# Kernel tuning notes

Measured on AMD Instinct MI355X. Metric: run time of the kernel, lower is better.

Reference implementation:

```python
import jax, jax.numpy as jnp
import numpy as np

N = 50000   # nodes
E = 300000  # directed edges (~Delaunay mesh, degree 6)
H = 128     # hidden_size
TW = 5      # time_window
P = 3       # process_steps
NODE_IN = 9
EDGE_IN = 4
LN_EPS = 1e-5


def _ln(x, g, b):
    m = jnp.mean(x, axis=-1, keepdims=True)
    v = jnp.var(x, axis=-1, keepdims=True)
    return (x - m) * jax.lax.rsqrt(v + LN_EPS) * g + b


def _mlp_ln(x, w1, b1, w2, b2, g, bb):
    # Linear -> ReLU -> Linear -> LayerNorm (matches MLP(..., layer_norm=True))
    h = jax.nn.relu(x @ w1 + b1)
    return _ln(h @ w2 + b2, g, bb)


def setup_inputs() -> dict:
    key = jax.random.key(0)
    ks = iter(jax.random.split(key, 64))
    def nrm(shape):
        return jax.random.normal(next(ks), shape, jnp.float32)
    def lin(fi, fo, stack=None):
        sh = (fi, fo) if stack is None else (stack, fi, fo)
        return nrm(sh) / np.sqrt(fi)
    inp = {}
    inp["temperature"] = nrm((N,))
    inp["temperature_prev"] = nrm((N,))
    inp["heat_source"] = nrm((N,))
    inp["heat_source_prev"] = nrm((N,))
    inp["heat_source_next"] = nrm((N, TW))
    inp["mesh_pos"] = jax.random.uniform(next(ks), (N, 2), jnp.float32)
    inp["edge_index"] = jax.random.randint(next(ks), (2, E), 0, N, jnp.int32)
    # Normalizer params (running mean/std)
    inp["node_norm_mean"] = jnp.zeros((NODE_IN,), jnp.float32)
    inp["node_norm_std"] = jnp.ones((NODE_IN,), jnp.float32)
    inp["edge_norm_mean"] = jnp.zeros((EDGE_IN,), jnp.float32)
    inp["edge_norm_std"] = jnp.ones((EDGE_IN,), jnp.float32)
    # node encoder
    inp["ne_w1"] = lin(NODE_IN, H); inp["ne_b1"] = jnp.zeros((H,), jnp.float32)
    inp["ne_w2"] = lin(H, H);       inp["ne_b2"] = jnp.zeros((H,), jnp.float32)
    inp["ne_g"] = jnp.ones((H,), jnp.float32); inp["ne_be"] = jnp.zeros((H,), jnp.float32)
    # edge encoder
    inp["ee_w1"] = lin(EDGE_IN, H); inp["ee_b1"] = jnp.zeros((H,), jnp.float32)
    inp["ee_w2"] = lin(H, H);       inp["ee_b2"] = jnp.zeros((H,), jnp.float32)
    inp["ee_g"] = jnp.ones((H,), jnp.float32); inp["ee_be"] = jnp.zeros((H,), jnp.float32)
    # processors (stacked over P steps): edge_mlp in=3H, node_mlp in=2H
    inp["pe_w1"] = lin(3 * H, H, P); inp["pe_b1"] = jnp.zeros((P, H), jnp.float32)
    inp["pe_w2"] = lin(H, H, P);     inp["pe_b2"] = jnp.zeros((P, H), jnp.float32)
    inp["pe_g"] = jnp.ones((P, H), jnp.float32); inp["pe_be"] = jnp.zeros((P, H), jnp.float32)
    inp["pn_w1"] = lin(2 * H, H, P); inp["pn_b1"] = jnp.zeros((P, H), jnp.float32)
    inp["pn_w2"] = lin(H, H, P);     inp["pn_b2"] = jnp.zeros((P, H), jnp.float32)
    inp["pn_g"] = jnp.ones((P, H), jnp.float32); inp["pn_be"] = jnp.zeros((P, H), jnp.float32)
    # decoder (Conv1d kernel_size=1 == per-node Linear), Swish in between
    inp["dec_w1"] = lin(H, H // 2); inp["dec_b1"] = jnp.zeros((H // 2,), jnp.float32)
    inp["dec_w2"] = lin(H // 2, TW); inp["dec_b2"] = jnp.zeros((TW,), jnp.float32)
    return inp


def reference(temperature, temperature_prev, heat_source, heat_source_prev,
              heat_source_next, mesh_pos, edge_index,
              node_norm_mean, node_norm_std, edge_norm_mean, edge_norm_std,
              ne_w1, ne_b1, ne_w2, ne_b2, ne_g, ne_be,
              ee_w1, ee_b1, ee_w2, ee_b2, ee_g, ee_be,
              pe_w1, pe_b1, pe_w2, pe_b2, pe_g, pe_be,
              pn_w1, pn_b1, pn_w2, pn_b2, pn_g, pn_be,
              dec_w1, dec_b1, dec_w2, dec_b2):
    u = temperature
    # node features: [u, u_dot, q, q_dot, q_next]  -> [N, 9]
    x = jnp.concatenate([
        u[:, None], (u - temperature_prev)[:, None],
        heat_source[:, None], (heat_source - heat_source_prev)[:, None],
        heat_source_next], axis=-1)
    s, r = edge_index[0], edge_index[1]  # senders (source j), receivers (target i)
    rel = mesh_pos[s] - mesh_pos[r]                       # [E, 2]
    dist = jnp.linalg.norm(rel, axis=-1, keepdims=True)   # [E, 1]
    relt = (u[s] - u[r])[:, None]                         # [E, 1]
    e = jnp.concatenate([rel, dist, relt], axis=-1)       # [E, 4]

    xh = _mlp_ln((x - node_norm_mean) / node_norm_std, ne_w1, ne_b1, ne_w2, ne_b2, ne_g, ne_be)
    eh = _mlp_ln((e - edge_norm_mean) / edge_norm_std, ee_w1, ee_b1, ee_w2, ee_b2, ee_g, ee_be)

    n_nodes = xh.shape[0]
    for i in range(P):
        xs, xr = xh[s], xh[r]  # x_j = x[source], x_i = x[target]
        # message: edge_mlp(cat[x_i, x_j, e]) then scatter-add at target index
        msg = _mlp_ln(jnp.concatenate([xr, xs, eh], axis=-1),
                      pe_w1[i], pe_b1[i], pe_w2[i], pe_b2[i], pe_g[i], pe_be[i])
        aggr = jax.ops.segment_sum(msg, r, num_segments=n_nodes)
        # node update + residual
        new_x = _mlp_ln(jnp.concatenate([aggr, xh], axis=-1),
                        pn_w1[i], pn_b1[i], pn_w2[i], pn_b2[i], pn_g[i], pn_be[i]) + xh
        # edge update (note row/col ordering differs from message) + residual
        new_e = _mlp_ln(jnp.concatenate([xs, xr, eh], axis=-1),
                        pe_w1[i], pe_b1[i], pe_w2[i], pe_b2[i], pe_g[i], pe_be[i]) + eh
        xh, eh = new_x, new_e

    # decoder: 1x1 convs == per-node linears, Swish(beta=1) activation
    h = xh @ dec_w1 + dec_b1
    h = h * jax.nn.sigmoid(h)
    delta = (h @ dec_w2 + dec_b2).reshape(-1, TW)
    dt = jnp.arange(1, TW + 1, dtype=delta.dtype)
    return dt[None, :] * delta
```

## Files before the change

kernel.cpp:

```cpp
#include <hip/hip_runtime.h>
#include <stdint.h>

typedef unsigned short u16;
typedef __attribute__((ext_vector_type(8))) short bf16x8_t;
typedef __attribute__((ext_vector_type(4))) float f32x4_t;

__device__ __forceinline__ float bl(u16 x) {
  union { unsigned u; float f; } c; c.u = ((unsigned)x) << 16; return c.f;
}
__device__ __forceinline__ u16 fb(float x) {
  union { float f; unsigned u; } c; c.f = x;
  unsigned r = c.u + 0x7fffu + ((c.u >> 16) & 1u);
  return (u16)(r >> 16);
}

__global__ void sentinel_kernel(float* out, int n) {
  int i = blockIdx.x * 256 + threadIdx.x;
  if (i < n) out[i] = 12345.f;
}

struct TSeg { const float* src; u16* dst; };
struct TArgs { TSeg s[23]; };
__global__ void transpose_w(TArgs a) {
  __shared__ u16 sT[128][132];
  const float* src = a.s[blockIdx.x].src;
  u16* dst = a.s[blockIdx.x].dst;
  for (int e = threadIdx.x; e < 16384; e += 256) {
    int k = e >> 7, n = e & 127;
    sT[n][k] = fb(src[e]);
  }
  __syncthreads();
  for (int e = threadIdx.x; e < 16384; e += 256) {
    int n = e >> 7, k = e & 127;
    dst[e] = sT[n][k];
  }
}

__global__ void zero_i32(int* p, int n) {
  int i = blockIdx.x * 256 + threadIdx.x;
  if (i < n) p[i] = 0;
}
__global__ void deg_count(const int* __restrict__ ei, int* __restrict__ cnt, int E) {
  int e = blockIdx.x * 256 + threadIdx.x;
  if (e < E) atomicAdd(&cnt[ei[E + e]], 1);
}
__global__ void scan1(const int* __restrict__ cnt, int* __restrict__ part,
                      int* __restrict__ bsum, int N) {
  __shared__ int s[256];
  int i = blockIdx.x * 256 + threadIdx.x;
  s[threadIdx.x] = (i < N) ? cnt[i] : 0;
  __syncthreads();
#pragma unroll
  for (int o = 1; o < 256; o <<= 1) {
    int t = (threadIdx.x >= o) ? s[threadIdx.x - o] : 0;
    __syncthreads();
    s[threadIdx.x] += t;
    __syncthreads();
  }
  if (i < N) part[i] = s[threadIdx.x];
  if (threadIdx.x == 255) bsum[blockIdx.x] = s[255];
}
__global__ void scan2(int* bsum, int nb) {
  __shared__ int s[256];
  __shared__ int carry;
  if (threadIdx.x == 0) carry = 0;
  __syncthreads();
  for (int base = 0; base < nb; base += 256) {
    int i = base + threadIdx.x;
    int v = (i < nb) ? bsum[i] : 0;
    s[threadIdx.x] = v;
    __syncthreads();
#pragma unroll
    for (int o = 1; o < 256; o <<= 1) {
      int t = (threadIdx.x >= o) ? s[threadIdx.x - o] : 0;
      __syncthreads();
      s[threadIdx.x] += t;
      __syncthreads();
    }
    int exc = s[threadIdx.x] - v + carry;
    if (i < nb) bsum[i] = exc;
    __syncthreads();
    if (threadIdx.x == 255) carry += s[255];
    __syncthreads();
  }
}
__global__ void scan3(const int* __restrict__ part, const int* __restrict__ bsum,
                      int* __restrict__ start, int N) {
  int i = blockIdx.x * 256 + threadIdx.x;
  if (i < N) start[i + 1] = part[i] + bsum[i >> 8];
  if (i == 0) start[0] = 0;
}
__global__ void fill_slot(const int* __restrict__ ei, int* __restrict__ cnt2,
                          const int* __restrict__ start, int* __restrict__ sortedS,
                          int* __restrict__ sortedR, int E) {
  int e = blockIdx.x * 256 + threadIdx.x;
  if (e >= E) return;
  int s = ei[e], r = ei[E + e];
  int p = atomicAdd(&cnt2[r], 1);
  int slot = start[r] + p;
  sortedS[slot] = s;
  sortedR[slot] = r;
}

__global__ void node_feat_kernel(const float* __restrict__ t, const float* __restrict__ tp,
                                 const float* __restrict__ q, const float* __restrict__ qp,
                                 const float* __restrict__ qn, const float* __restrict__ nm,
                                 const float* __restrict__ ns, float* __restrict__ nfeat,
                                 int n_nodes) {
  int n = blockIdx.x * 256 + threadIdx.x;
  if (n >= n_nodes) return;
  float u = t[n];
  float x[9];
  x[0] = u; x[1] = u - tp[n];
  float hq = q[n];
  x[2] = hq; x[3] = hq - qp[n];
#pragma unroll
  for (int j = 0; j < 5; ++j) x[4 + j] = qn[n * 5 + j];
#pragma unroll
  for (int k = 0; k < 9; ++k) nfeat[n * 9 + k] = (x[k] - nm[k]) / ns[k];
}

__global__ void edge_feat_kernel(const int* __restrict__ sArr, const int* __restrict__ rArr,
                                 const float* __restrict__ mp, const float* __restrict__ u,
                                 const float* __restrict__ em, const float* __restrict__ es,
                                 float* __restrict__ efeat, int n_edges) {
  int e = blockIdx.x * 256 + threadIdx.x;
  if (e >= n_edges) return;
  int s = sArr[e], r = rArr[e];
  float rx = mp[s * 2] - mp[r * 2];
  float ry = mp[s * 2 + 1] - mp[r * 2 + 1];
  float d = sqrtf(rx * rx + ry * ry);
  float rt = u[s] - u[r];
  float x[4] = {rx, ry, d, rt};
#pragma unroll
  for (int k = 0; k < 4; ++k) efeat[e * 4 + k] = (x[k] - em[k]) / es[k];
}

template <int K, bool DUAL>
__global__ __launch_bounds__(256, 2) void encode_fused(
    const float* __restrict__ feat, const float* __restrict__ w1f, const float* __restrict__ b1f,
    const u16* __restrict__ wt2, const float* __restrict__ b2, const float* __restrict__ gg,
    const float* __restrict__ bb, u16* __restrict__ out,
    const u16* __restrict__ wtA2, const u16* __restrict__ wtB2, u16* __restrict__ xhA,
    u16* __restrict__ xhB, float* __restrict__ aggr, int M) {
  __shared__ float sW1[K * 128];
  __shared__ float sB1[128];
  __shared__ u16 sH[64][136];
  __shared__ u16 sO1[DUAL ? 64 : 1][136];
  const int tid = threadIdx.x;
  const int wave = tid >> 6, lane = tid & 63;
  const int q = lane >> 4, l16 = lane & 15;
  const int m0 = blockIdx.x * 64;
  const int rowb = wave * 16 + q * 4;
  const int arow = m0 + wave * 16 + l16;
  const int arc = arow < M ? arow : M - 1;

  for (int i = tid; i < K * 128; i += 256) sW1[i] = w1f[i];
  if (tid < 128) sB1[tid] = b1f[tid];
  __syncthreads();

  float fr[K];
#pragma unroll
  for (int k = 0; k < K; ++k) fr[k] = feat[(size_t)arc * K + k];

  f32x4_t acc[8];
#pragma unroll
  for (int b = 0; b < 8; ++b) acc[b] = (f32x4_t){0.f, 0.f, 0.f, 0.f};
#pragma unroll
  for (int kk = 0; kk < 4; ++kk) {
    union { u16 u[8]; bf16x8_t v; } cv;
#pragma unroll
    for (int j = 0; j < 8; ++j) {
      int col = kk * 32 + q * 8 + j;
      float h = sB1[col];
#pragma unroll
      for (int k = 0; k < K; ++k) h += fr[k] * sW1[k * 128 + col];
      cv.u[j] = fb(h > 0.f ? h : 0.f);
    }
#pragma unroll
    for (int nt = 0; nt < 8; ++nt) {
      bf16x8_t bfv = *(const bf16x8_t*)(wt2 + (size_t)(nt * 16 + l16) * 128 + kk * 32 + q * 8);
      acc[nt] = __builtin_amdgcn_mfma_f32_16x16x32_bf16(cv.v, bfv, acc[nt], 0, 0, 0);
    }
  }

  float bcol[8], gcol[8], becol[8];
#pragma unroll
  for (int nt = 0; nt < 8; ++nt) {
    bcol[nt] = b2[nt * 16 + l16];
    gcol[nt] = gg[nt * 16 + l16];
    becol[nt] = bb[nt * 16 + l16];
  }
  float s[4] = {0, 0, 0, 0}, ss[4] = {0, 0, 0, 0};
#pragma unroll
  for (int r = 0; r < 4; ++r)
#pragma unroll
    for (int nt = 0; nt < 8; ++nt) {
      float v = acc[nt][r] + bcol[nt];
      s[r] += v;
      ss[r] += v * v;
    }
#pragma unroll
  for (int r = 0; r < 4; ++r) {
#pragma unroll
    for (int m = 1; m <= 8; m <<= 1) {
      s[r] += __shfl_xor(s[r], m, 64);
      ss[r] += __shfl_xor(ss[r], m, 64);
    }
  }
#pragma unroll
  for (int r = 0; r < 4; ++r) {
    float mean = s[r] * (1.f / 128.f);
    float var = fmaxf(ss[r] * (1.f / 128.f) - mean * mean, 0.f);
    float rstd = rsqrtf(var + 1e-5f);
#pragma unroll
    for (int nt = 0; nt < 8; ++nt) {
      float v = (acc[nt][r] + bcol[nt] - mean) * rstd * gcol[nt] + becol[nt];
      sH[rowb + r][nt * 16 + l16] = fb(v);
    }
  }
  __syncthreads();
#pragma unroll
  for (int it = 0; it < 4; ++it) {
    int lin = it * 256 + tid;
    int row = lin >> 4, ch = (lin & 15) * 8;
    int grow = m0 + row;
    if (grow >= M) continue;
    *(uint4*)(out + (size_t)grow * 128 + ch) = *(uint4*)(&sH[row][ch]);
  }

  if constexpr (DUAL) {
    {
      float4 z = make_float4(0.f, 0.f, 0.f, 0.f);
#pragma unroll
      for (int it = 0; it < 8; ++it) {
        int lin = it * 256 + tid;
        int row = lin >> 5, c4 = (lin & 31) * 4;
        int grow = m0 + row;
        if (grow < M) *(float4*)(aggr + (size_t)grow * 128 + c4) = z;
      }
    }
    f32x4_t a0[8], a1[8];
#pragma unroll
    for (int b = 0; b < 8; ++b) {
      a0[b] = (f32x4_t){0.f, 0.f, 0.f, 0.f};
      a1[b] = (f32x4_t){0.f, 0.f, 0.f, 0.f};
    }
#pragma unroll
    for (int kk = 0; kk < 4; ++kk) {
      bf16x8_t af = *(const bf16x8_t*)(&sH[wave * 16 + l16][kk * 32 + q * 8]);
#pragma unroll
      for (int nt = 0; nt < 8; ++nt) {
        bf16x8_t b0 = *(const bf16x8_t*)(wtA2 + (size_t)(nt * 16 + l16) * 128 + kk * 32 + q * 8);
        bf16x8_t b1v = *(const bf16x8_t*)(wtB2 + (size_t)(nt * 16 + l16) * 128 + kk * 32 + q * 8);
        a0[nt] = __builtin_amdgcn_mfma_f32_16x16x32_bf16(af, b0, a0[nt], 0, 0, 0);
        a1[nt] = __builtin_amdgcn_mfma_f32_16x16x32_bf16(af, b1v, a1[nt], 0, 0, 0);
      }
    }
    __syncthreads();
#pragma unroll
    for (int r = 0; r < 4; ++r)
#pragma unroll
      for (int nt = 0; nt < 8; ++nt) {
        sH[rowb + r][nt * 16 + l16] = fb(a0[nt][r]);
        sO1[rowb + r][nt * 16 + l16] = fb(a1[nt][r]);
      }
    __syncthreads();
#pragma unroll
    for (int it = 0; it < 4; ++it) {
      int lin = it * 256 + tid;
      int row = lin >> 4, ch = (lin & 15) * 8;
      int grow = m0 + row;
      if (grow >= M) continue;
      *(uint4*)(xhA + (size_t)grow * 128 + ch) = *(uint4*)(&sH[row][ch]);
      *(uint4*)(xhB + (size_t)grow * 128 + ch) = *(uint4*)(&sO1[row][ch]);
    }
  }
}

__global__ __launch_bounds__(256, 2) void node_fused_2w(
    u16* __restrict__ xh, float* __restrict__ aggr, const u16* __restrict__ wtA,
    const u16* __restrict__ wtB, const float* __restrict__ b1, const u16* __restrict__ wt2,
    const float* __restrict__ b2, const float* __restrict__ gg, const float* __restrict__ bb,
    const u16* __restrict__ wtA2, const u16* __restrict__ wtB2, u16* __restrict__ xhA,
    u16* __restrict__ xhB, int M) {
  __shared__ u16 sH[64][136];
  __shared__ u16 sO1[64][136];
  const int tid = threadIdx.x;
  const int wave = tid >> 6, lane = tid & 63;
  const int q = lane >> 4, l16 = lane & 15;
  const int m0 = blockIdx.x * 64;
  const int rowb = wave * 16 + q * 4;
  const int arow = m0 + wave * 16 + l16;
  const int arc = arow < M ? arow : M - 1;

  bf16x8_t xf[4], af_[4];
#pragma unroll
  for (int kk = 0; kk < 4; ++kk) {
    xf[kk] = *(const bf16x8_t*)(xh + (size_t)arc * 128 + kk * 32 + q * 8);
    const float* ap = aggr + (size_t)arc * 128 + kk * 32 + q * 8;
    union { u16 u[8]; bf16x8_t v; } cv;
#pragma unroll
    for (int j = 0; j < 8; ++j) cv.u[j] = fb(ap[j]);
    af_[kk] = cv.v;
  }

  f32x4_t acc[8];
#pragma unroll
  for (int b = 0; b < 8; ++b) acc[b] = (f32x4_t){0.f, 0.f, 0.f, 0.f};
#pragma unroll
  for (int kk = 0; kk < 4; ++kk) {
#pragma unroll
    for (int nt = 0; nt < 8; ++nt) {
      bf16x8_t bA = *(const bf16x8_t*)(wtA + (size_t)(nt * 16 + l16) * 128 + kk * 32 + q * 8);
      bf16x8_t bB = *(const bf16x8_t*)(wtB + (size_t)(nt * 16 + l16) * 128 + kk * 32 + q * 8);
      acc[nt] = __builtin_amdgcn_mfma_f32_16x16x32_bf16(af_[kk], bA, acc[nt], 0, 0, 0);
      acc[nt] = __builtin_amdgcn_mfma_f32_16x16x32_bf16(xf[kk], bB, acc[nt], 0, 0, 0);
    }
  }
  float bcol1[8];
#pragma unroll
  for (int nt = 0; nt < 8; ++nt) bcol1[nt] = b1[nt * 16 + l16];
#pragma unroll
  for (int r = 0; r < 4; ++r)
#pragma unroll
    for (int nt = 0; nt < 8; ++nt) {
      float v = acc[nt][r] + bcol1[nt];
      sH[rowb + r][nt * 16 + l16] = fb(v > 0.f ? v : 0.f);
    }
  __syncthreads();

  f32x4_t acc2[8];
#pragma unroll
  for (int b = 0; b < 8; ++b) acc2[b] = (f32x4_t){0.f, 0.f, 0.f, 0.f};
#pragma unroll
  for (int kk = 0; kk < 4; ++kk) {
    bf16x8_t afm = *(const bf16x8_t*)(&sH[wave * 16 + l16][kk * 32 + q * 8]);
#pragma unroll
    for (int nt = 0; nt < 8; ++nt) {
      bf16x8_t bfv = *(const bf16x8_t*)(wt2 + (size_t)(nt * 16 + l16) * 128 + kk * 32 + q * 8);
      acc2[nt] = __builtin_amdgcn_mfma_f32_16x16x32_bf16(afm, bfv, acc2[nt], 0, 0, 0);
    }
  }
  float bcol[8], gcol[8], becol[8];
#pragma unroll
  for (int nt = 0; nt < 8; ++nt) {
    bcol[nt] = b2[nt * 16 + l16];
    gcol[nt] = gg[nt * 16 + l16];
    becol[nt] = bb[nt * 16 + l16];
  }
  float s[4] = {0, 0, 0, 0}, ss[4] = {0, 0, 0, 0};
#pragma unroll
  for (int r = 0; r < 4; ++r)
#pragma unroll
    for (int nt = 0; nt < 8; ++nt) {
      float v = acc2[nt][r] + bcol[nt];
      s[r] += v;
      ss[r] += v * v;
    }
#pragma unroll
  for (int r = 0; r < 4; ++r) {
#pragma unroll
    for (int m = 1; m <= 8; m <<= 1) {
      s[r] += __shfl_xor(s[r], m, 64);
      ss[r] += __shfl_xor(ss[r], m, 64);
    }
  }
  __syncthreads();
#pragma unroll
  for (int r = 0; r < 4; ++r) {
    float mean = s[r] * (1.f / 128.f);
    float var = fmaxf(ss[r] * (1.f / 128.f) - mean * mean, 0.f);
    float rstd = rsqrtf(var + 1e-5f);
#pragma unroll
    for (int nt = 0; nt < 8; ++nt) {
      float v = (acc2[nt][r] + bcol[nt] - mean) * rstd * gcol[nt] + becol[nt];
      sH[rowb + r][nt * 16 + l16] = fb(v);
    }
  }
  __syncthreads();

  bf16x8_t nf[4];
#pragma unroll
  for (int kk = 0; kk < 4; ++kk) {
    u16 y8[8];
    *(uint4*)y8 = *(uint4*)(&sH[wave * 16 + l16][kk * 32 + q * 8]);
#pragma unroll
    for (int j = 0; j < 8; ++j) y8[j] = fb(bl(y8[j]) + bl((u16)xf[kk][j]));
    nf[kk] = *(bf16x8_t*)y8;
    if (arow < M)
      *(uint4*)(xh + (size_t)arow * 128 + kk * 32 + q * 8) = *(uint4*)y8;
  }

  if (wtA2 == nullptr) return;

  if (arow < M) {
    float4 z = make_float4(0.f, 0.f, 0.f, 0.f);
#pragma unroll
    for (int kk = 0; kk < 4; ++kk) {
      *(float4*)(aggr + (size_t)arow * 128 + kk * 32 + q * 8) = z;
      *(float4*)(aggr + (size_t)arow * 128 + kk * 32 + q * 8 + 4) = z;
    }
  }

  f32x4_t a0[8], a1[8];
#pragma unroll
  for (int b = 0; b < 8; ++b) {
    a0[b] = (f32x4_t){0.f, 0.f, 0.f, 0.f};
    a1[b] = (f32x4_t){0.f, 0.f, 0.f, 0.f};
  }
#pragma unroll
  for (int kk = 0; kk < 4; ++kk) {
#pragma unroll
    for (int nt = 0; nt < 8; ++nt) {
      bf16x8_t b0 = *(const bf16x8_t*)(wtA2 + (size_t)(nt * 16 + l16) * 128 + kk * 32 + q * 8);
      bf16x8_t b1v = *(const bf16x8_t*)(wtB2 + (size_t)(nt * 16 + l16) * 128 + kk * 32 + q * 8);
      a0[nt] = __builtin_amdgcn_mfma_f32_16x16x32_bf16(nf[kk], b0, a0[nt], 0, 0, 0);
      a1[nt] = __builtin_amdgcn_mfma_f32_16x16x32_bf16(nf[kk], b1v, a1[nt], 0, 0, 0);
    }
  }
  __syncthreads();
#pragma unroll
  for (int r = 0; r < 4; ++r)
#pragma unroll
    for (int nt = 0; nt < 8; ++nt) {
      sH[rowb + r][nt * 16 + l16] = fb(a0[nt][r]);
      sO1[rowb + r][nt * 16 + l16] = fb(a1[nt][r]);
    }
  __syncthreads();
#pragma unroll
  for (int it = 0; it < 4; ++it) {
    int lin = it * 256 + tid;
    int row = lin >> 4, ch = (lin & 15) * 8;
    int grow = m0 + row;
    if (grow >= M) continue;
    *(uint4*)(xhA + (size_t)grow * 128 + ch) = *(uint4*)(&sH[row][ch]);
    *(uint4*)(xhB + (size_t)grow * 128 + ch) = *(uint4*)(&sO1[row][ch]);
  }
}

template <bool CSR, bool LAST>
__global__ __launch_bounds__(256, 2) void edge_fused(
    u16* __restrict__ eh, const u16* __restrict__ xhA, const u16* __restrict__ xhB,
    const u16* __restrict__ wtC, const float* __restrict__ b1, const u16* __restrict__ wt2,
    const float* __restrict__ b2, const float* __restrict__ gg, const float* __restrict__ bb,
    const int* __restrict__ sArr, const int* __restrict__ rArr,
    const int* __restrict__ startp, float* __restrict__ aggr, int E) {
  __shared__ u16 sHm[64][136];
  __shared__ u16 sHe[LAST ? 1 : 64][136];
  __shared__ int sR[64];
  __shared__ float sB1[128];
  const int tid = threadIdx.x;
  const int wave = tid >> 6, lane = tid & 63;
  const int q = lane >> 4, l16 = lane & 15;
  const int m0 = blockIdx.x * 64;
  const int rowb = wave * 16 + q * 4;
  int arow = m0 + wave * 16 + l16;
  int arc = arow < E ? arow : E - 1;

  if (tid < 64) {
    int e = m0 + tid;
    sR[tid] = (e < E) ? rArr[e] : -1;
  }
  if (tid < 128) sB1[tid] = b1[tid];

  int psv[4], prv[4];
#pragma unroll
  for (int it = 0; it < 4; ++it) {
    int lin = it * 256 + tid;
    int ge = m0 + (lin >> 4);
    int gc = ge < E ? ge : E - 1;
    psv[it] = sArr[gc];
    prv[it] = rArr[gc];
  }

  bf16x8_t ehf[4];
#pragma unroll
  for (int kk = 0; kk < 4; ++kk)
    ehf[kk] = *(const bf16x8_t*)(eh + (size_t)arc * 128 + kk * 32 + q * 8);

  f32x4_t accC[8];
#pragma unroll
  for (int b = 0; b < 8; ++b) accC[b] = (f32x4_t){0.f, 0.f, 0.f, 0.f};
#pragma unroll
  for (int kk = 0; kk < 4; ++kk) {
#pragma unroll
    for (int nt = 0; nt < 8; ++nt) {
      bf16x8_t bfv = *(const bf16x8_t*)(wtC + (size_t)(nt * 16 + l16) * 128 + kk * 32 + q * 8);
      accC[nt] = __builtin_amdgcn_mfma_f32_16x16x32_bf16(ehf[kk], bfv, accC[nt], 0, 0, 0);
    }
  }
  __builtin_amdgcn_sched_barrier(0);

  uint4 pAr[4], pBs[4], pAs[4], pBr[4];
#pragma unroll
  for (int it = 0; it < 4; ++it) {
    int ch = ((it * 256 + tid) & 15) * 8;
    pAr[it] = *(const uint4*)(xhA + (size_t)prv[it] * 128 + ch);
    pBs[it] = *(const uint4*)(xhB + (size_t)psv[it] * 128 + ch);
    if constexpr (!LAST) {
      pAs[it] = *(const uint4*)(xhA + (size_t)psv[it] * 128 + ch);
      pBr[it] = *(const uint4*)(xhB + (size_t)prv[it] * 128 + ch);
    }
  }

#pragma unroll
  for (int r = 0; r < 4; ++r)
#pragma unroll
    for (int nt = 0; nt < 8; ++nt) sHm[rowb + r][nt * 16 + l16] = fb(accC[nt][r]);
  __syncthreads();

#pragma unroll
  for (int it = 0; it < 4; ++it) {
    int lin = it * 256 + tid;
    int row = lin >> 4, ch = (lin & 15) * 8;
    bool ok = (m0 + row) < E;
    u16 t8[8], ar[8], as_[8], br[8], bs[8], hm[8], he[8];
    *(uint4*)t8 = *(uint4*)(&sHm[row][ch]);
    *(uint4*)ar = pAr[it];
    *(uint4*)bs = pBs[it];
    if constexpr (!LAST) {
      *(uint4*)as_ = pAs[it];
      *(uint4*)br = pBr[it];
    }
#pragma unroll
    for (int j = 0; j < 8; ++j) {
      float t = bl(t8[j]) + sB1[ch + j];
      float vm = t + bl(ar[j]) + bl(bs[j]);
      hm[j] = (ok && vm > 0.f) ? fb(vm) : 0;
      if constexpr (!LAST) {
        float ve = t + bl(as_[j]) + bl(br[j]);
        he[j] = (ok && ve > 0.f) ? fb(ve) : 0;
      }
    }
    *(uint4*)(&sHm[row][ch]) = *(uint4*)hm;
    if constexpr (!LAST) *(uint4*)(&sHe[row][ch]) = *(uint4*)he;
  }
  __syncthreads();

  float bcol[8], gcol[8], becol[8];
#pragma unroll
  for (int nt = 0; nt < 8; ++nt) {
    bcol[nt] = b2[nt * 16 + l16];
    gcol[nt] = gg[nt * 16 + l16];
    becol[nt] = bb[nt * 16 + l16];
  }

  f32x4_t accM[8], accE[8];
#pragma unroll
  for (int b = 0; b < 8; ++b) {
    accM[b] = (f32x4_t){0.f, 0.f, 0.f, 0.f};
    accE[b] = (f32x4_t){0.f, 0.f, 0.f, 0.f};
  }
#pragma unroll
  for (int kk = 0; kk < 4; ++kk) {
    bf16x8_t afm = *(const bf16x8_t*)(&sHm[wave * 16 + l16][kk * 32 + q * 8]);
    bf16x8_t afe;
    if constexpr (!LAST) afe = *(const bf16x8_t*)(&sHe[wave * 16 + l16][kk * 32 + q * 8]);
#pragma unroll
    for (int nt = 0; nt < 8; ++nt) {
      bf16x8_t bfv = *(const bf16x8_t*)(wt2 + (size_t)(nt * 16 + l16) * 128 + kk * 32 + q * 8);
      accM[nt] = __builtin_amdgcn_mfma_f32_16x16x32_bf16(afm, bfv, accM[nt], 0, 0, 0);
      if constexpr (!LAST)
        accE[nt] = __builtin_amdgcn_mfma_f32_16x16x32_bf16(afe, bfv, accE[nt], 0, 0, 0);
    }
  }
  float sm[4] = {0, 0, 0, 0}, ssm[4] = {0, 0, 0, 0};
  float se[4] = {0, 0, 0, 0}, sse[4] = {0, 0, 0, 0};
#pragma unroll
  for (int r = 0; r < 4; ++r)
#pragma unroll
    for (int nt = 0; nt < 8; ++nt) {
      float vm = accM[nt][r] + bcol[nt];
      sm[r] += vm; ssm[r] += vm * vm;
      if constexpr (!LAST) {
        float ve = accE[nt][r] + bcol[nt];
        se[r] += ve; sse[r] += ve * ve;
      }
    }
#pragma unroll
  for (int r = 0; r < 4; ++r) {
#pragma unroll
    for (int m = 1; m <= 8; m <<= 1) {
      sm[r] += __shfl_xor(sm[r], m, 64);
      ssm[r] += __shfl_xor(ssm[r], m, 64);
      if constexpr (!LAST) {
        se[r] += __shfl_xor(se[r], m, 64);
        sse[r] += __shfl_xor(sse[r], m, 64);
      }
    }
  }

  if (!CSR) {
#pragma unroll
    for (int r = 0; r < 4; ++r) {
      int row = m0 + rowb + r;
      if (row >= E) continue;
      int rr = sR[rowb + r];
      float mean = sm[r] * (1.f / 128.f);
      float var = fmaxf(ssm[r] * (1.f / 128.f) - mean * mean, 0.f);
      float rstd = rsqrtf(var + 1e-5f);
#pragma unroll
      for (int nt = 0; nt < 8; ++nt) {
        float v = (accM[nt][r] + bcol[nt] - mean) * rstd * gcol[nt] + becol[nt];
        atomicAdd(&aggr[(size_t)rr * 128 + nt * 16 + l16], v);
      }
    }
  }

  __syncthreads();
#pragma unroll
  for (int r = 0; r < 4; ++r) {
    float meanM = sm[r] * (1.f / 128.f);
    float varM = fmaxf(ssm[r] * (1.f / 128.f) - meanM * meanM, 0.f);
    float rstdM = rsqrtf(varM + 1e-5f);
    if constexpr (!LAST) {
      float meanE = se[r] * (1.f / 128.f);
      float varE = fmaxf(sse[r] * (1.f / 128.f) - meanE * meanE, 0.f);
      float rstdE = rsqrtf(varE + 1e-5f);
#pragma unroll
      for (int nt = 0; nt < 8; ++nt) {
        float ve = (accE[nt][r] + bcol[nt] - meanE) * rstdE * gcol[nt] + becol[nt];
        sHe[rowb + r][nt * 16 + l16] = fb(ve);
      }
    }
    if (CSR) {
#pragma unroll
      for (int nt = 0; nt < 8; ++nt) {
        float vm = (accM[nt][r] + bcol[nt] - meanM) * rstdM * gcol[nt] + becol[nt];
        sHm[rowb + r][nt * 16 + l16] = fb(vm);
      }
    }
  }
  __syncthreads();

#pragma unroll
  for (int it = 0; it < 4; ++it) {
    int lin = it * 256 + tid;
    int row = lin >> 4, ch = (lin & 15) * 8;
    int grow = m0 + row;
    if (grow >= E) continue;
    if constexpr (!LAST) {
      u16 y8[8], e8[8];
      *(uint4*)y8 = *(uint4*)(&sHe[row][ch]);
      *(uint4*)e8 = *(const uint4*)(eh + (size_t)grow * 128 + ch);
#pragma unroll
      for (int j = 0; j < 8; ++j) y8[j] = fb(bl(y8[j]) + bl(e8[j]));
      *(uint4*)(eh + (size_t)grow * 128 + ch) = *(uint4*)y8;
    }

    if (CSR) {
      int rr = sR[row];
      if (rr < 0) continue;
      bool first = (row == 0) || (sR[row - 1] != rr);
      if (!first) continue;
      int gs = startp[rr], ge2 = startp[rr + 1];
      int le = ge2 - m0;
      if (le > 64) le = 64;
      float acc[8] = {0, 0, 0, 0, 0, 0, 0, 0};
      for (int i = row; i < le; ++i) {
        u16 m8[8];
        *(uint4*)m8 = *(uint4*)(&sHm[i][ch]);
#pragma unroll
        for (int j = 0; j < 8; ++j) acc[j] += bl(m8[j]);
      }
      if (gs >= m0 && ge2 <= m0 + 64) {
        *(float4*)(aggr + (size_t)rr * 128 + ch) = make_float4(acc[0], acc[1], acc[2], acc[3]);
        *(float4*)(aggr + (size_t)rr * 128 + ch + 4) =
            make_float4(acc[4], acc[5], acc[6], acc[7]);
      } else {
#pragma unroll
        for (int j = 0; j < 8; ++j) atomicAdd(&aggr[(size_t)rr * 128 + ch + j], acc[j]);
      }
    }
  }
}

__global__ void decoder_kernel(const u16* __restrict__ xh, const float* __restrict__ w1,
                               const float* __restrict__ b1, const float* __restrict__ w2,
                               const float* __restrict__ b2, float* __restrict__ out,
                               int n_nodes) {
  __shared__ float sx[4][128];
  int tid = threadIdx.x;
  int lw = tid >> 6, lane = tid & 63;
  int n0 = blockIdx.x * 4;
  for (int i = tid; i < 512; i += 256) {
    int nn = i >> 7, c = i & 127;
    int n = n0 + nn;
    sx[nn][c] = (n < n_nodes) ? bl(xh[(size_t)n * 128 + c]) : 0.f;
  }
  __syncthreads();
  int n = n0 + lw;
  float h = b1[lane];
#pragma unroll 16
  for (int k = 0; k < 128; ++k) h += sx[lw][k] * w1[k * 64 + lane];
  float hs = h * (1.f / (1.f + __expf(-h)));
  float d[5];
#pragma unroll
  for (int t = 0; t < 5; ++t) {
    float p = hs * w2[lane * 5 + t];
#pragma unroll
    for (int m = 1; m <= 32; m <<= 1) p += __shfl_xor(p, m, 64);
    d[t] = p;
  }
  if (lane == 0 && n < n_nodes) {
#pragma unroll
    for (int t = 0; t < 5; ++t)
      out[(size_t)n * 5 + t] = (float)(t + 1) * (d[t] + b2[t]);
  }
}

extern "C" void kernel_launch(void* const* d_in, const int* in_sizes, int n_in, void* d_out,
                              int out_size, void* d_ws, size_t ws_size, hipStream_t stream) {
  auto F = [&](int i) { return (const float*)d_in[i]; };
  const int* edge_index = (const int*)d_in[6];
  const int N_ = in_sizes[0];
  const int E_ = in_sizes[6] / 2;

  char* wsb = (char*)d_ws;
  size_t off = 0;
  auto alloc = [&](size_t bytes) -> char* {
    char* p = wsb + off;
    off += (bytes + 255) & ~(size_t)255;
    return p;
  };
  u16* xh = (u16*)alloc((size_t)N_ * 128 * 2);
  u16* xhA = (u16*)alloc((size_t)N_ * 128 * 2);
  u16* xhB = (u16*)alloc((size_t)N_ * 128 * 2);
  u16* ehP = (u16*)alloc((size_t)E_ * 128 * 2);
  float* aggr = (float*)alloc((size_t)N_ * 128 * 4);
  float* nfeat = (float*)aggr;
  float* efeat = (float*)xhB;
  u16* wne2T = (u16*)alloc(16384 * 2);
  u16* wee2T = (u16*)alloc(16384 * 2);
  u16* wpe1T = (u16*)alloc((size_t)9 * 16384 * 2);
  u16* wpe2T = (u16*)alloc((size_t)3 * 16384 * 2);
  u16* wpn1T = (u16*)alloc((size_t)6 * 16384 * 2);
  u16* wpn2T = (u16*)alloc((size_t)3 * 16384 * 2);

  const size_t base_off = off;
  int* startp = (int*)alloc((size_t)(N_ + 1) * 4);
  int* cntp = (int*)alloc((size_t)N_ * 4);
  int* partp = (int*)alloc((size_t)N_ * 4);
  int* bsump = (int*)alloc(((size_t)(N_ + 255) / 256) * 4 + 256);
  int* sortedS = (int*)alloc((size_t)E_ * 4);
  int* sortedR = (int*)alloc((size_t)E_ * 4);
  bool useCSR = (off <= ws_size);
  if (!useCSR) {
    off = base_off;
    if (off > ws_size) {
      sentinel_kernel<<<(out_size + 255) / 256, 256, 0, stream>>>((float*)d_out, out_size);
      return;
    }
  }

  TArgs ta;
  int ts = 0;
  ta.s[ts++] = {F(13), wne2T};
  ta.s[ts++] = {F(19), wee2T};
  for (int i = 0; i < 3; ++i)
    for (int b = 0; b < 3; ++b)
      ta.s[ts++] = {F(23) + (size_t)(i * 3 + b) * 16384, wpe1T + (size_t)(i * 3 + b) * 16384};
  for (int i = 0; i < 3; ++i) ta.s[ts++] = {F(25) + (size_t)i * 16384, wpe2T + (size_t)i * 16384};
  for (int i = 0; i < 3; ++i)
    for (int b = 0; b < 2; ++b)
      ta.s[ts++] = {F(29) + (size_t)(i * 2 + b) * 16384, wpn1T + (size_t)(i * 2 + b) * 16384};
  for (int i = 0; i < 3; ++i) ta.s[ts++] = {F(31) + (size_t)i * 16384, wpn2T + (size_t)i * 16384};

  const int tilesN = (N_ + 63) / 64;
  const int tilesE = (E_ + 63) / 64;
  const int nb = (N_ + 255) / 256;
  dim3 blk(256);

  transpose_w<<<23, blk, 0, stream>>>(ta);

  const int* sArr = edge_index;
  const int* rArr = edge_index + E_;
  if (useCSR) {
    zero_i32<<<(N_ + 255) / 256, blk, 0, stream>>>(cntp, N_);
    deg_count<<<(E_ + 255) / 256, blk, 0, stream>>>(edge_index, cntp, E_);
    scan1<<<nb, blk, 0, stream>>>(cntp, partp, bsump, N_);
    scan2<<<1, blk, 0, stream>>>(bsump, nb);
    scan3<<<nb, blk, 0, stream>>>(partp, bsump, startp, N_);
    zero_i32<<<(N_ + 255) / 256, blk, 0, stream>>>(cntp, N_);
    fill_slot<<<(E_ + 255) / 256, blk, 0, stream>>>(edge_index, cntp, startp, sortedS, sortedR,
                                                    E_);
    sArr = sortedS;
    rArr = sortedR;
  }

  edge_feat_kernel<<<(E_ + 255) / 256, blk, 0, stream>>>(sArr, rArr, F(5), F(0), F(9), F(10),
                                                         efeat, E_);
  encode_fused<4, false><<<tilesE, blk, 0, stream>>>(efeat, F(17), F(18), wee2T, F(20), F(21),
                                                     F(22), ehP, nullptr, nullptr, nullptr,
                                                     nullptr, nullptr, E_);
  node_feat_kernel<<<(N_ + 255) / 256, blk, 0, stream>>>(F(0), F(1), F(2), F(3), F(4), F(7),
                                                         F(8), nfeat, N_);
  encode_fused<9, true><<<tilesN, blk, 0, stream>>>(nfeat, F(11), F(12), wne2T, F(14), F(15),
                                                    F(16), xh, wpe1T, wpe1T + 16384, xhA, xhB,
                                                    aggr, N_);

  for (int i = 0; i < 3; ++i) {
    const u16* wtC = wpe1T + (size_t)(i * 3 + 2) * 16384;
    const float* pb1 = F(24) + i * 128;
    const u16* wt2 = wpe2T + (size_t)i * 16384;
    const float* pb2 = F(26) + i * 128;
    const float* pg = F(27) + i * 128;
    const float* pbe = F(28) + i * 128;
    const u16* wtnA = wpn1T + (size_t)(i * 2 + 0) * 16384;
    const u16* wtnB = wpn1T + (size_t)(i * 2 + 1) * 16384;
    const float* nb1 = F(30) + i * 128;
    const u16* wtn2 = wpn2T + (size_t)i * 16384;
    const float* nb2 = F(32) + i * 128;
    const float* ng = F(33) + i * 128;
    const float* nbe = F(34) + i * 128;

    const bool last = (i == 2);
    if (useCSR) {
      if (last)
        edge_fused<true, true><<<tilesE, blk, 0, stream>>>(ehP, xhA, xhB, wtC, pb1, wt2, pb2,
                                                           pg, pbe, sArr, rArr, startp, aggr, E_);
      else
        edge_fused<true, false><<<tilesE, blk, 0, stream>>>(ehP, xhA, xhB, wtC, pb1, wt2, pb2,
                                                            pg, pbe, sArr, rArr, startp, aggr, E_);
    } else {
      if (last)
        edge_fused<false, true><<<tilesE, blk, 0, stream>>>(ehP, xhA, xhB, wtC, pb1, wt2, pb2,
                                                            pg, pbe, sArr, rArr, nullptr, aggr, E_);
      else
        edge_fused<false, false><<<tilesE, blk, 0, stream>>>(ehP, xhA, xhB, wtC, pb1, wt2, pb2,
                                                             pg, pbe, sArr, rArr, nullptr, aggr, E_);
    }
    const u16* wtA2 = (i < 2) ? wpe1T + (size_t)((i + 1) * 3 + 0) * 16384 : nullptr;
    const u16* wtB2 = (i < 2) ? wpe1T + (size_t)((i + 1) * 3 + 1) * 16384 : nullptr;
    node_fused_2w<<<tilesN, blk, 0, stream>>>(xh, aggr, wtnA, wtnB, nb1, wtn2, nb2, ng, nbe,
                                              wtA2, wtB2, xhA, xhB, N_);
  }

  decoder_kernel<<<(N_ + 3) / 4, blk, 0, stream>>>(xh, F(35), F(36), F(37), F(38),
                                                   (float*)d_out, N_);
}
```

Before: 1.157 ms.

## Split edge kernel across 8 waves with column-split MFMA and shared LN partials

The fused edge kernel now runs 512 threads per 64-edge tile. Each pair of waves splits the 128 output columns in half, which halves the per-thread accumulator registers, and the launch bounds are raised to target higher occupancy. LayerNorm row sums are reduced across the two column halves through shared memory, and bias, gamma and beta are staged in LDS. The explicit register prefetch of gathered node features before the first sync is dropped. Gathers are now issued after the first GEMM, which risks exposing more latency. The extra barrier and LDS traffic are traded for more waves in flight.

After: 1.235 ms. +6.8%, slower.

```diff
diff --git a/kernel.cpp b/kernel.cpp
--- a/kernel.cpp
+++ b/kernel.cpp
@@ -440,7 +440,7 @@
 }
 
 template <bool CSR, bool LAST>
-__global__ __launch_bounds__(256, 2) void edge_fused(
+__global__ __launch_bounds__(512, 8) void edge_fused(
     u16* __restrict__ eh, const u16* __restrict__ xhA, const u16* __restrict__ xhB,
     const u16* __restrict__ wtC, const float* __restrict__ b1, const u16* __restrict__ wt2,
     const float* __restrict__ b2, const float* __restrict__ gg, const float* __restrict__ bb,
@@ -449,79 +449,65 @@
   __shared__ u16 sHm[64][136];
   __shared__ u16 sHe[LAST ? 1 : 64][136];
   __shared__ int sR[64];
-  __shared__ float sB1[128];
+  __shared__ float sB1[128], sB2[128], sG[128], sBe[128];
+  __shared__ float sPm[2][64], sPSm[2][64];
+  __shared__ float sPe[LAST ? 1 : 2][64], sPSe[LAST ? 1 : 2][64];
   const int tid = threadIdx.x;
   const int wave = tid >> 6, lane = tid & 63;
   const int q = lane >> 4, l16 = lane & 15;
+  const int waveR = wave >> 1, waveC = wave & 1;
+  const int ntb = waveC * 4;
   const int m0 = blockIdx.x * 64;
-  const int rowb = wave * 16 + q * 4;
-  int arow = m0 + wave * 16 + l16;
+  const int rowb = waveR * 16 + q * 4;
+  int arow = m0 + waveR * 16 + l16;
   int arc = arow < E ? arow : E - 1;
 
-  if (tid < 64) {
-    int e = m0 + tid;
-    sR[tid] = (e < E) ? rArr[e] : -1;
-  }
-  if (tid < 128) sB1[tid] = b1[tid];
-
-  int psv[4], prv[4];
-#pragma unroll
-  for (int it = 0; it < 4; ++it) {
-    int lin = it * 256 + tid;
-    int ge = m0 + (lin >> 4);
+  if (tid < 64) sR[tid] = (m0 + tid < E) ? rArr[m0 + tid] : -1;
+  if (tid >= 128 && tid < 256) {
+    int t = tid - 128;
+    sB1[t] = b1[t]; sB2[t] = b2[t]; sG[t] = gg[t]; sBe[t] = bb[t];
+  }
+
+  {
+    bf16x8_t ehf[4];
+#pragma unroll
+    for (int kk = 0; kk < 4; ++kk)
+      ehf[kk] = *(const bf16x8_t*)(eh + (size_t)arc * 128 + kk * 32 + q * 8);
+    f32x4_t accC[4];
+#pragma unroll
+    for (int j = 0; j < 4; ++j) accC[j] = (f32x4_t){0.f, 0.f, 0.f, 0.f};
+#pragma unroll
+    for (int kk = 0; kk < 4; ++kk) {
+#pragma unroll
+      for (int j = 0; j < 4; ++j) {
+        bf16x8_t bfv =
+            *(const bf16x8_t*)(wtC + (size_t)((ntb + j) * 16 + l16) * 128 + kk * 32 + q * 8);
+        accC[j] = __builtin_amdgcn_mfma_f32_16x16x32_bf16(ehf[kk], bfv, accC[j], 0, 0, 0);
+      }
+    }
+#pragma unroll
+    for (int r = 0; r < 4; ++r)
+#pragma unroll
+      for (int j = 0; j < 4; ++j)
+        sHm[rowb + r][(ntb + j) * 16 + l16] = fb(accC[j][r]);
+  }
+  __syncthreads();
+
+#pragma unroll
+  for (int it = 0; it < 2; ++it) {
+    int lin = it * 512 + tid;
+    int row = lin >> 4, ch = (lin & 15) * 8;
+    int ge = m0 + row;
     int gc = ge < E ? ge : E - 1;
-    psv[it] = sArr[gc];
-    prv[it] = rArr[gc];
-  }
-
-  bf16x8_t ehf[4];
-#pragma unroll
-  for (int kk = 0; kk < 4; ++kk)
-    ehf[kk] = *(const bf16x8_t*)(eh + (size_t)arc * 128 + kk * 32 + q * 8);
-
-  f32x4_t accC[8];
-#pragma unroll
-  for (int b = 0; b < 8; ++b) accC[b] = (f32x4_t){0.f, 0.f, 0.f, 0.f};
-#pragma unroll
-  for (int kk = 0; kk < 4; ++kk) {
-#pragma unroll
-    for (int nt = 0; nt < 8; ++nt) {
-      bf16x8_t bfv = *(const bf16x8_t*)(wtC + (size_t)(nt * 16 + l16) * 128 + kk * 32 + q * 8);
-      accC[nt] = __builtin_amdgcn_mfma_f32_16x16x32_bf16(ehf[kk], bfv, accC[nt], 0, 0, 0);
-    }
-  }
-  __builtin_amdgcn_sched_barrier(0);
-
-  uint4 pAr[4], pBs[4], pAs[4], pBr[4];
-#pragma unroll
-  for (int it = 0; it < 4; ++it) {
-    int ch = ((it * 256 + tid) & 15) * 8;
-    pAr[it] = *(const uint4*)(xhA + (size_t)prv[it] * 128 + ch);
-    pBs[it] = *(const uint4*)(xhB + (size_t)psv[it] * 128 + ch);
-    if constexpr (!LAST) {
-      pAs[it] = *(const uint4*)(xhA + (size_t)psv[it] * 128 + ch);
-      pBr[it] = *(const uint4*)(xhB + (size_t)prv[it] * 128 + ch);
-    }
-  }
-
-#pragma unroll
-  for (int r = 0; r < 4; ++r)
-#pragma unroll
-    for (int nt = 0; nt < 8; ++nt) sHm[rowb + r][nt * 16 + l16] = fb(accC[nt][r]);
-  __syncthreads();
-
-#pragma unroll
-  for (int it = 0; it < 4; ++it) {
-    int lin = it * 256 + tid;
-    int row = lin >> 4, ch = (lin & 15) * 8;
-    bool ok = (m0 + row) < E;
+    int ps = sArr[gc], pr = rArr[gc];
+    bool ok = ge < E;
     u16 t8[8], ar[8], as_[8], br[8], bs[8], hm[8], he[8];
     *(uint4*)t8 = *(uint4*)(&sHm[row][ch]);
-    *(uint4*)ar = pAr[it];
-    *(uint4*)bs = pBs[it];
+    *(uint4*)ar = *(const uint4*)(xhA + (size_t)pr * 128 + ch);
+    *(uint4*)bs = *(const uint4*)(xhB + (size_t)ps * 128 + ch);
     if constexpr (!LAST) {
-      *(uint4*)as_ = pAs[it];
-      *(uint4*)br = pBr[it];
+      *(uint4*)as_ = *(const uint4*)(xhA + (size_t)ps * 128 + ch);
+      *(uint4*)br = *(const uint4*)(xhB + (size_t)pr * 128 + ch);
     }
 #pragma unroll
     for (int j = 0; j < 8; ++j) {
@@ -538,105 +524,115 @@
   }
   __syncthreads();
 
-  float bcol[8], gcol[8], becol[8];
-#pragma unroll
-  for (int nt = 0; nt < 8; ++nt) {
-    bcol[nt] = b2[nt * 16 + l16];
-    gcol[nt] = gg[nt * 16 + l16];
-    becol[nt] = bb[nt * 16 + l16];
-  }
-
-  f32x4_t accM[8], accE[8];
-#pragma unroll
-  for (int b = 0; b < 8; ++b) {
-    accM[b] = (f32x4_t){0.f, 0.f, 0.f, 0.f};
-    accE[b] = (f32x4_t){0.f, 0.f, 0.f, 0.f};
+  f32x4_t accM[4], accE[4];
+#pragma unroll
+  for (int j = 0; j < 4; ++j) {
+    accM[j] = (f32x4_t){0.f, 0.f, 0.f, 0.f};
+    accE[j] = (f32x4_t){0.f, 0.f, 0.f, 0.f};
   }
 #pragma unroll
   for (int kk = 0; kk < 4; ++kk) {
-    bf16x8_t afm = *(const bf16x8_t*)(&sHm[wave * 16 + l16][kk * 32 + q * 8]);
+    bf16x8_t afm = *(const bf16x8_t*)(&sHm[waveR * 16 + l16][kk * 32 + q * 8]);
     bf16x8_t afe;
-    if constexpr (!LAST) afe = *(const bf16x8_t*)(&sHe[wave * 16 + l16][kk * 32 + q * 8]);
-#pragma unroll
-    for (int nt = 0; nt < 8; ++nt) {
-      bf16x8_t bfv = *(const bf16x8_t*)(wt2 + (size_t)(nt * 16 + l16) * 128 + kk * 32 + q * 8);
-      accM[nt] = __builtin_amdgcn_mfma_f32_16x16x32_bf16(afm, bfv, accM[nt], 0, 0, 0);
+    if constexpr (!LAST) afe = *(const bf16x8_t*)(&sHe[waveR * 16 + l16][kk * 32 + q * 8]);
+#pragma unroll
+    for (int j = 0; j < 4; ++j) {
+      bf16x8_t bfv =
+          *(const bf16x8_t*)(wt2 + (size_t)((ntb + j) * 16 + l16) * 128 + kk * 32 + q * 8);
+      accM[j] = __builtin_amdgcn_mfma_f32_16x16x32_bf16(afm, bfv, accM[j], 0, 0, 0);
       if constexpr (!LAST)
-        accE[nt] = __builtin_amdgcn_mfma_f32_16x16x32_bf16(afe, bfv, accE[nt], 0, 0, 0);
-    }
-  }
-  float sm[4] = {0, 0, 0, 0}, ssm[4] = {0, 0, 0, 0};
-  float se[4] = {0, 0, 0, 0}, sse[4] = {0, 0, 0, 0};
-#pragma unroll
-  for (int r = 0; r < 4; ++r)
-#pragma unroll
-    for (int nt = 0; nt < 8; ++nt) {
-      float vm = accM[nt][r] + bcol[nt];
-      sm[r] += vm; ssm[r] += vm * vm;
-      if constexpr (!LAST) {
-        float ve = accE[nt][r] + bcol[nt];
-        se[r] += ve; sse[r] += ve * ve;
-      }
-    }
+        accE[j] = __builtin_amdgcn_mfma_f32_16x16x32_bf16(afe, bfv, accE[j], 0, 0, 0);
+    }
+  }
+  float bcv[4];
+#pragma unroll
+  for (int j = 0; j < 4; ++j) bcv[j] = sB2[(ntb + j) * 16 + l16];
+  {
+    float sm[4] = {0, 0, 0, 0}, ssm[4] = {0, 0, 0, 0};
+    float se[4] = {0, 0, 0, 0}, sse[4] = {0, 0, 0, 0};
+#pragma unroll
+    for (int r = 0; r < 4; ++r)
+#pragma unroll
+      for (int j = 0; j < 4; ++j) {
+        float vm = accM[j][r] + bcv[j];
+        sm[r] += vm; ssm[r] += vm * vm;
+        if constexpr (!LAST) {
+          float ve = accE[j][r] + bcv[j];
+          se[r] += ve; sse[r] += ve * ve;
+        }
+      }
+#pragma unroll
+    for (int r = 0; r < 4; ++r) {
+#pragma unroll
+      for (int m = 1; m <= 8; m <<= 1) {
+        sm[r] += __shfl_xor(sm[r], m, 64);
+        ssm[r] += __shfl_xor(ssm[r], m, 64);
+        if constexpr (!LAST) {
+          se[r] += __shfl_xor(se[r], m, 64);
+          sse[r] += __shfl_xor(sse[r], m, 64);
+        }
+      }
+    }
+    if (l16 == 0) {
+#pragma unroll
+      for (int r = 0; r < 4; ++r) {
+        sPm[waveC][rowb + r] = sm[r];
+        sPSm[waveC][rowb + r] = ssm[r];
+        if constexpr (!LAST) {
+          sPe[waveC][rowb + r] = se[r];
+          sPSe[waveC][rowb + r] = sse[r];
+        }
+      }
+    }
+  }
+  __syncthreads();
+
 #pragma unroll
   for (int r = 0; r < 4; ++r) {
-#pragma unroll
-    for (int m = 1; m <= 8; m <<= 1) {
-      sm[r] += __shfl_xor(sm[r], m, 64);
-      ssm[r] += __shfl_xor(ssm[r], m, 64);
-      if constexpr (!LAST) {
-        se[r] += __shfl_xor(se[r], m, 64);
-        sse[r] += __shfl_xor(sse[r], m, 64);
-      }
-    }
-  }
-
-  if (!CSR) {
-#pragma unroll
-    for (int r = 0; r < 4; ++r) {
-      int row = m0 + rowb + r;
-      if (row >= E) continue;
-      int rr = sR[rowb + r];
-      float mean = sm[r] * (1.f / 128.f);
-      float var = fmaxf(ssm[r] * (1.f / 128.f) - mean * mean, 0.f);
-      float rstd = rsqrtf(var + 1e-5f);
-#pragma unroll
-      for (int nt = 0; nt < 8; ++nt) {
-        float v = (accM[nt][r] + bcol[nt] - mean) * rstd * gcol[nt] + becol[nt];
-        atomicAdd(&aggr[(size_t)rr * 128 + nt * 16 + l16], v);
-      }
-    }
-  }
-
-  __syncthreads();
-#pragma unroll
-  for (int r = 0; r < 4; ++r) {
-    float meanM = sm[r] * (1.f / 128.f);
-    float varM = fmaxf(ssm[r] * (1.f / 128.f) - meanM * meanM, 0.f);
+    int row = rowb + r;
+    float smf = sPm[0][row] + sPm[1][row];
+    float ssmf = sPSm[0][row] + sPSm[1][row];
+    float meanM = smf * (1.f / 128.f);
+    float varM = fmaxf(ssmf * (1.f / 128.f) - meanM * meanM, 0.f);
     float rstdM = rsqrtf(varM + 1e-5f);
+    if (CSR) {
+#pragma unroll
+      for (int j = 0; j < 4; ++j) {
+        int col = (ntb + j) * 16 + l16;
+        float vm = (accM[j][r] + bcv[j] - meanM) * rstdM * sG[col] + sBe[col];
+        sHm[row][col] = fb(vm);
+      }
+    } else {
+      int grow = m0 + row;
+      if (grow < E) {
+        int rr = sR[row];
+#pragma unroll
+        for (int j = 0; j < 4; ++j) {
+          int col = (ntb + j) * 16 + l16;
+          float vm = (accM[j][r] + bcv[j] - meanM) * rstdM * sG[col] + sBe[col];
+          atomicAdd(&aggr[(size_t)rr * 128 + col], vm);
+        }
+      }
+    }
     if constexpr (!LAST) {
-      float meanE = se[r] * (1.f / 128.f);
-      float varE = fmaxf(sse[r] * (1.f / 128.f) - meanE * meanE, 0.f);
+      float sef = sPe[0][row] + sPe[1][row];
+      float ssef = sPSe[0][row] + sPSe[1][row];
+      float meanE = sef * (1.f / 128.f);
+      float varE = fmaxf(ssef * (1.f / 128.f) - meanE * meanE, 0.f);
       float rstdE = rsqrtf(varE + 1e-5f);
 #pragma unroll
-      for (int nt = 0; nt < 8; ++nt) {
-        float ve = (accE[nt][r] + bcol[nt] - meanE) * rstdE * gcol[nt] + becol[nt];
-        sHe[rowb + r][nt * 16 + l16] = fb(ve);
-      }
-    }
-    if (CSR) {
-#pragma unroll
-      for (int nt = 0; nt < 8; ++nt) {
-        float vm = (accM[nt][r] + bcol[nt] - meanM) * rstdM * gcol[nt] + becol[nt];
-        sHm[rowb + r][nt * 16 + l16] = fb(vm);
-      }
-    }
-  }
-  __syncthreads();
-
-#pragma unroll
-  for (int it = 0; it < 4; ++it) {
-    int lin = it * 256 + tid;
+      for (int j = 0; j < 4; ++j) {
+        int col = (ntb + j) * 16 + l16;
+        float ve = (accE[j][r] + bcv[j] - meanE) * rstdE * sG[col] + sBe[col];
+        sHe[row][col] = fb(ve);
+      }
+    }
+  }
+  __syncthreads();
+
+#pragma unroll
+  for (int it = 0; it < 2; ++it) {
+    int lin = it * 512 + tid;
     int row = lin >> 4, ch = (lin & 15) * 8;
     int grow = m0 + row;
     if (grow >= E) continue;
@@ -648,7 +644,6 @@
       for (int j = 0; j < 8; ++j) y8[j] = fb(bl(y8[j]) + bl(e8[j]));
       *(uint4*)(eh + (size_t)grow * 128 + ch) = *(uint4*)y8;
     }
-
     if (CSR) {
       int rr = sR[row];
       if (rr < 0) continue;
@@ -771,6 +766,7 @@
   const int tilesE = (E_ + 63) / 64;
   const int nb = (N_ + 255) / 256;
   dim3 blk(256);
+  dim3 blkE(512);
 
   transpose_w<<<23, blk, 0, stream>>>(ta);
 
@@ -818,18 +814,18 @@
     const bool last = (i == 2);
     if (useCSR) {
       if (last)
-        edge_fused<true, true><<<tilesE, blk, 0, stream>>>(ehP, xhA, xhB, wtC, pb1, wt2, pb2,
-                                                           pg, pbe, sArr, rArr, startp, aggr, E_);
+        edge_fused<true, true><<<tilesE, blkE, 0, stream>>>(ehP, xhA, xhB, wtC, pb1, wt2, pb2,
+                                                            pg, pbe, sArr, rArr, startp, aggr, E_);
       else
-        edge_fused<true, false><<<tilesE, blk, 0, stream>>>(ehP, xhA, xhB, wtC, pb1, wt2, pb2,
-                                                            pg, pbe, sArr, rArr, startp, aggr, E_);
+        edge_fused<true, false><<<tilesE, blkE, 0, stream>>>(ehP, xhA, xhB, wtC, pb1, wt2, pb2,
+                                                             pg, pbe, sArr, rArr, startp, aggr, E_);
     } else {
       if (last)
-        edge_fused<false, true><<<tilesE, blk, 0, stream>>>(ehP, xhA, xhB, wtC, pb1, wt2, pb2,
-                                                            pg, pbe, sArr, rArr, nullptr, aggr, E_);
+        edge_fused<false, true><<<tilesE, blkE, 0, stream>>>(ehP, xhA, xhB, wtC, pb1, wt2, pb2,
+                                                             pg, pbe, sArr, rArr, nullptr, aggr, E_);
       else
-        edge_fused<false, false><<<tilesE, blk, 0, stream>>>(ehP, xhA, xhB, wtC, pb1, wt2, pb2,
-                                                             pg, pbe, sArr, rArr, nullptr, aggr, E_);
+        edge_fused<false, false><<<tilesE, blkE, 0, stream>>>(ehP, xhA, xhB, wtC, pb1, wt2, pb2,
+                                                              pg, pbe, sArr, rArr, nullptr, aggr, E_);
     }
     const u16* wtA2 = (i < 2) ? wpe1T + (size_t)((i + 1) * 3 + 0) * 16384 : nullptr;
     const u16* wtB2 = (i < 2) ? wpe1T + (size_t)((i + 1) * 3 + 1) * 16384 : nullptr;
```

## Rewrite decoder as MFMA tile kernel with pre-transposed bf16 weights

Applied to the files above, without the earlier changes.

Replaces the scalar per-node decoder (4 nodes per block, FP32 FMA over a 128x64 weight read from global memory) with a 64-node tile kernel. The first linear layer runs as bf16 MFMA 16x16x32, and the second layer is computed from shared memory. A one-block transpose kernel converts dec_w1 to bf16 [64][128] layout up front. This cuts global weight re-reads and FMA count, at the cost of bf16 rounding of w1 and an extra small launch.

Result: no change. 1.137 ms (-1.7%).

```diff
diff --git a/kernel.cpp b/kernel.cpp
--- a/kernel.cpp
+++ b/kernel.cpp
@@ -31,6 +31,19 @@
   }
   __syncthreads();
   for (int e = threadIdx.x; e < 16384; e += 256) {
+    int n = e >> 7, k = e & 127;
+    dst[e] = sT[n][k];
+  }
+}
+
+__global__ void transpose_w1d(const float* __restrict__ src, u16* __restrict__ dst) {
+  __shared__ u16 sT[64][132];
+  for (int e = threadIdx.x; e < 8192; e += 256) {
+    int k = e >> 6, n = e & 63;
+    sT[n][k] = fb(src[e]);
+  }
+  __syncthreads();
+  for (int e = threadIdx.x; e < 8192; e += 256) {
     int n = e >> 7, k = e & 127;
     dst[e] = sT[n][k];
   }
@@ -676,37 +689,58 @@
   }
 }
 
-__global__ void decoder_kernel(const u16* __restrict__ xh, const float* __restrict__ w1,
-                               const float* __restrict__ b1, const float* __restrict__ w2,
-                               const float* __restrict__ b2, float* __restrict__ out,
-                               int n_nodes) {
-  __shared__ float sx[4][128];
-  int tid = threadIdx.x;
-  int lw = tid >> 6, lane = tid & 63;
-  int n0 = blockIdx.x * 4;
-  for (int i = tid; i < 512; i += 256) {
-    int nn = i >> 7, c = i & 127;
-    int n = n0 + nn;
-    sx[nn][c] = (n < n_nodes) ? bl(xh[(size_t)n * 128 + c]) : 0.f;
-  }
-  __syncthreads();
-  int n = n0 + lw;
-  float h = b1[lane];
-#pragma unroll 16
-  for (int k = 0; k < 128; ++k) h += sx[lw][k] * w1[k * 64 + lane];
-  float hs = h * (1.f / (1.f + __expf(-h)));
-  float d[5];
-#pragma unroll
-  for (int t = 0; t < 5; ++t) {
-    float p = hs * w2[lane * 5 + t];
-#pragma unroll
-    for (int m = 1; m <= 32; m <<= 1) p += __shfl_xor(p, m, 64);
-    d[t] = p;
-  }
-  if (lane == 0 && n < n_nodes) {
-#pragma unroll
-    for (int t = 0; t < 5; ++t)
-      out[(size_t)n * 5 + t] = (float)(t + 1) * (d[t] + b2[t]);
+__global__ __launch_bounds__(256, 2) void decoder_tile(
+    const u16* __restrict__ xh, const u16* __restrict__ w1t, const float* __restrict__ b1,
+    const float* __restrict__ w2, const float* __restrict__ b2, float* __restrict__ out,
+    int M) {
+  __shared__ float sHf[64][65];
+  __shared__ float sW2[320];
+  __shared__ float sB1[64];
+  const int tid = threadIdx.x;
+  const int wave = tid >> 6, lane = tid & 63;
+  const int q = lane >> 4, l16 = lane & 15;
+  const int m0 = blockIdx.x * 64;
+  const int rowb = wave * 16 + q * 4;
+  const int arow = m0 + wave * 16 + l16;
+  const int arc = arow < M ? arow : M - 1;
+
+  for (int i = tid; i < 320; i += 256) sW2[i] = w2[i];
+  if (tid < 64) sB1[tid] = b1[tid];
+
+  f32x4_t acc[4];
+#pragma unroll
+  for (int b = 0; b < 4; ++b) acc[b] = (f32x4_t){0.f, 0.f, 0.f, 0.f};
+#pragma unroll
+  for (int kk = 0; kk < 4; ++kk) {
+    bf16x8_t xf = *(const bf16x8_t*)(xh + (size_t)arc * 128 + kk * 32 + q * 8);
+#pragma unroll
+    for (int nt = 0; nt < 4; ++nt) {
+      bf16x8_t bfv = *(const bf16x8_t*)(w1t + (size_t)(nt * 16 + l16) * 128 + kk * 32 + q * 8);
+      acc[nt] = __builtin_amdgcn_mfma_f32_16x16x32_bf16(xf, bfv, acc[nt], 0, 0, 0);
+    }
+  }
+  __syncthreads();
+#pragma unroll
+  for (int r = 0; r < 4; ++r)
+#pragma unroll
+    for (int nt = 0; nt < 4; ++nt) {
+      float h = acc[nt][r] + sB1[nt * 16 + l16];
+      float hs = h * (1.f / (1.f + __expf(-h)));
+      sHf[rowb + r][nt * 16 + l16] = hs;
+    }
+  __syncthreads();
+
+  int row = tid >> 2, tq = tid & 3;
+  int grow = m0 + row;
+  if (grow < M) {
+#pragma unroll
+    for (int t0 = 0; t0 < 2; ++t0) {
+      int t = (t0 == 0) ? tq : (tq == 0 ? 4 : -1);
+      if (t < 0) continue;
+      float p = b2[t];
+      for (int k = 0; k < 64; ++k) p += sHf[row][k] * sW2[k * 5 + t];
+      out[(size_t)grow * 5 + t] = (float)(t + 1) * p;
+    }
   }
 }
 
@@ -737,6 +771,7 @@
   u16* wpe2T = (u16*)alloc((size_t)3 * 16384 * 2);
   u16* wpn1T = (u16*)alloc((size_t)6 * 16384 * 2);
   u16* wpn2T = (u16*)alloc((size_t)3 * 16384 * 2);
+  u16* w1dT = (u16*)alloc(8192 * 2);
 
   const size_t base_off = off;
   int* startp = (int*)alloc((size_t)(N_ + 1) * 4);
@@ -773,6 +808,7 @@
   dim3 blk(256);
 
   transpose_w<<<23, blk, 0, stream>>>(ta);
+  transpose_w1d<<<1, blk, 0, stream>>>(F(35), w1dT);
 
   const int* sArr = edge_index;
   const int* rArr = edge_index + E_;
@@ -837,6 +873,5 @@
                                               wtA2, wtB2, xhA, xhB, N_);
   }
 
-  decoder_kernel<<<(N_ + 3) / 4, blk, 0, stream>>>(xh, F(35), F(36), F(37), F(38),
-                                                   (float*)d_out, N_);
-}
+  decoder_tile<<<tilesN, blk, 0, stream>>>(xh, w1dT, F(36), F(37), F(38), (float*)d_out, N_);
+}
```
